# Optimization experiments

Measured on AMD Instinct MI355X. Metric: run time of the kernel, lower is better.

The kernel has to match this reference:

```python
import jax, jax.numpy as jnp
import numpy as np

B, P, V, E, F = 4, 8, 2048, 2048, 4096
BIG = 1e10  # stand-in for +inf that keeps gradients clean


def setup_inputs() -> dict:
    key = jax.random.key(0)
    ks = jax.random.split(key, 8)
    xs = jax.random.normal(ks[0], (B, V, 3), jnp.float32)
    # Projection matrices: random rows for x/y, third (depth) row kept near
    # [0,0,0,2] so the perspective divide is well conditioned for randn verts.
    pm = 0.5 * jax.random.normal(ks[1], (P, 3, 4), jnp.float32)
    pm = pm.at[:, 2, :3].set(0.01 * jax.random.normal(ks[2], (P, 3), jnp.float32))
    pm = pm.at[:, 2, 3].set(2.0)
    edgemaps = jax.random.normal(ks[3], (B, P, E, 2), jnp.float32)
    edgemap_lengths = jax.random.randint(ks[4], (B, P), E // 2, E + 1)
    boundary_mask = jax.random.randint(ks[5], (B, P, V), 0, 2).astype(bool)
    faces = jax.random.randint(ks[6], (B, F, 3), 0, V)
    target_volumes = 10.0 * jax.random.normal(ks[7], (B,), jnp.float32)
    return dict(xs=xs, projmatrices=pm, edgemaps=edgemaps,
                edgemap_lengths=edgemap_lengths, boundary_mask=boundary_mask,
                faces=faces, target_volumes=target_volumes)


def _silhouette_chamfer(xs, projmatrices, edgemaps, edgemap_lengths, boundary_mask):
    b, v, _ = xs.shape
    xh = jnp.concatenate([xs, jnp.ones((b, v, 1), xs.dtype)], axis=-1)  # [B,V,4]
    proj = jnp.einsum('pij,bvj->bpvi', projmatrices, xh)               # [B,P,V,3]
    pts = proj[..., :2] / proj[..., 2:3]                               # [B,P,V,2]
    e = edgemaps.shape[2]
    d2 = (jnp.sum(pts * pts, -1)[..., :, None]
          + jnp.sum(edgemaps * edgemaps, -1)[..., None, :]
          - 2.0 * jnp.einsum('bpvc,bpec->bpve', pts, edgemaps))
    yvalid = jnp.arange(e)[None, None, :] < edgemap_lengths[..., None]  # [B,P,E]
    d2 = jnp.where(yvalid[:, :, None, :], d2, jnp.asarray(BIG, d2.dtype))
    mins = jnp.min(d2, axis=-1)                                        # [B,P,V]
    xm = boundary_mask.astype(d2.dtype)
    # point_reduction='mean' over valid boundary points per projection,
    # batch_reduction='mean' over the P projections of each mesh.
    per_proj = jnp.sum(mins * xm, -1) / jnp.maximum(jnp.sum(xm, -1), 1.0)  # [B,P]
    return jnp.mean(per_proj, axis=-1)                                 # [B]


def _volume_constraint(xs, faces, target_volumes):
    b = xs.shape[0]
    fv = xs[jnp.arange(b)[:, None, None], faces]   # [B,F,3,3] gather face verts
    v0, v1, v2 = fv[:, :, 0], fv[:, :, 1], fv[:, :, 2]
    face_vols = jnp.sum(jnp.cross(v0, v1) * v2, axis=-1) / 6.0  # [B,F]
    vols = jnp.abs(jnp.sum(face_vols, axis=-1))                 # scatter-add per mesh
    return (vols - target_volumes) ** 2                          # [B]


def reference(xs, projmatrices, edgemaps, edgemap_lengths, boundary_mask, faces, target_volumes):
    chamfer = _silhouette_chamfer(xs, projmatrices, edgemaps, edgemap_lengths, boundary_mask)
    vol_error = _volume_constraint(xs, faces, target_volumes)
    return chamfer, vol_error
```

## Files before the change

kernel.cpp:

```cpp
#include <hip/hip_runtime.h>

#define NB 4
#define NP 8
#define NV 2048
#define NE 2048
#define NF 4096
#define BIGV 1.0e10f
#define NCOMBO (NB * NP)
#define NSPAN 16
#define NVC 16
#define VC 128
#define NBLK (NCOMBO * NVC)
#define SSTRIDE 132
#define PPAD 132


typedef float f32x2 __attribute__((ext_vector_type(2)));

__device__ __forceinline__ f32x2 pk_fma(f32x2 a, f32x2 b, f32x2 c) {
    f32x2 d;
    asm("v_pk_fma_f32 %0, %1, %2, %3" : "=v"(d) : "v"(a), "v"(b), "v"(c));
    return d;
}

__global__ __launch_bounds__(256) void fused_all(
    const float* __restrict__ xs, const float* __restrict__ pm,
    const float* __restrict__ edgemaps, const int* __restrict__ elen,
    const int* __restrict__ faces, const void* __restrict__ maskp,
    float* __restrict__ spart, float* __restrict__ cpart,
    float* __restrict__ volpart)
{
    __shared__ __align__(16) float s_ex[NSPAN * SSTRIDE];
    __shared__ __align__(16) float s_ey[NSPAN * SSTRIDE];
    __shared__ __align__(16) float s_e2[NSPAN * SSTRIDE];
    __shared__ __align__(16) float part[NSPAN * PPAD];
    __shared__ float reds[2], redc[2];
    const int tid = threadIdx.x;
    const int bid = blockIdx.x;
    const int combo  = bid >> 4;
    const int vchunk = bid & 15;
    const int b = combo >> 3;
    const int p = combo & 7;

    const int len = elen[combo];
    const float4* emapf4 = (const float4*)(edgemaps + (size_t)combo * NE * 2);
    #pragma unroll
    for (int j = 0; j < 2; j++) {
        const int q = tid + (j << 8);
        const float4 f0 = emapf4[2 * q];
        const float4 f1 = emapf4[2 * q + 1];
        float ex[4] = { f0.x, f0.z, f1.x, f1.z };
        float ey[4] = { f0.y, f0.w, f1.y, f1.w };
        float e2[4];
        const int e0 = q << 2;
        #pragma unroll
        for (int k = 0; k < 4; k++) {
            if (e0 + k < len) {
                e2[k] = ex[k] * ex[k] + ey[k] * ey[k];
            } else {
                ex[k] = 0.0f; ey[k] = 0.0f; e2[k] = BIGV;
            }
        }
        const int sp = q >> 5, pr = (q & 31) << 2;
        *(float4*)&s_ex[sp * SSTRIDE + pr] = make_float4(ex[0], ex[1], ex[2], ex[3]);
        *(float4*)&s_ey[sp * SSTRIDE + pr] = make_float4(ey[0], ey[1], ey[2], ey[3]);
        *(float4*)&s_e2[sp * SSTRIDE + pr] = make_float4(e2[0], e2[1], e2[2], e2[3]);
    }

    const float* M = pm + p * 12;
    const float m00 = M[0], m01 = M[1], m02 = M[2],  m03 = M[3];
    const float m10 = M[4], m11 = M[5], m12 = M[6],  m13 = M[7];
    const float m20 = M[8], m21 = M[9], m22 = M[10], m23 = M[11];

    const int vgroup = tid & 15;
    const int span   = tid >> 4;
    const int v0     = vchunk * VC + (vgroup << 3);

    float c24[24];
    {
        const float4* xv = (const float4*)(xs + ((size_t)b * NV + v0) * 3);
        #pragma unroll
        for (int j = 0; j < 6; j++) ((float4*)c24)[j] = xv[j];
    }
    f32x2 px2[8], py2[8];
    float v2[8], mn[8];
    #pragma unroll
    for (int i = 0; i < 8; i++) {
        const float x = c24[3 * i], y = c24[3 * i + 1], z = c24[3 * i + 2];
        const float r0 = m00 * x + m01 * y + m02 * z + m03;
        const float r1 = m10 * x + m11 * y + m12 * z + m13;
        const float r2 = m20 * x + m21 * y + m22 * z + m23;
        const float inv = 1.0f / r2;
        const float px = r0 * inv;
        const float py = r1 * inv;
        const float ax = -2.0f * px, ay = -2.0f * py;
        px2[i].x = ax; px2[i].y = ax;
        py2[i].x = ay; py2[i].y = ay;
        v2[i]  = px * px + py * py;
        mn[i]  = 3.0e38f;
    }

    float fvol = 0.0f;
    if (tid < 32) {
        const int f = (bid << 5) + tid;
        const int* fc = faces + (size_t)f * 3;
        const int i0 = fc[0], i1 = fc[1], i2 = fc[2];
        const float* xb = xs + (size_t)(f >> 12) * NV * 3;
        const float ax = xb[i0 * 3], ay = xb[i0 * 3 + 1], az = xb[i0 * 3 + 2];
        const float bx = xb[i1 * 3], by = xb[i1 * 3 + 1], bz = xb[i1 * 3 + 2];
        const float cx = xb[i2 * 3], cy = xb[i2 * 3 + 1], cz = xb[i2 * 3 + 2];
        const float crx = ay * bz - az * by;
        const float cry = az * bx - ax * bz;
        const float crz = ax * by - ay * bx;
        fvol = (crx * cx + cry * cy + crz * cz) * (1.0f / 6.0f);
    }
    __syncthreads();

    const float* bx = s_ex + span * SSTRIDE;
    const float* by = s_ey + span * SSTRIDE;
    const float* b2 = s_e2 + span * SSTRIDE;
    #pragma unroll 2
    for (int k = 0; k < 32; k++) {
        const float4 ex4 = *(const float4*)(bx + 4 * k);
        const float4 ey4 = *(const float4*)(by + 4 * k);
        const float4 e24 = *(const float4*)(b2 + 4 * k);
        f32x2 exA, exB, eyA, eyB, e2A, e2B;
        exA.x = ex4.x; exA.y = ex4.y;  exB.x = ex4.z; exB.y = ex4.w;
        eyA.x = ey4.x; eyA.y = ey4.y;  eyB.x = ey4.z; eyB.y = ey4.w;
        e2A.x = e24.x; e2A.y = e24.y;  e2B.x = e24.z; e2B.y = e24.w;
        #pragma unroll
        for (int i = 0; i < 8; i++) {
            const f32x2 dA = pk_fma(py2[i], eyA, pk_fma(px2[i], exA, e2A));
            const f32x2 dB = pk_fma(py2[i], eyB, pk_fma(px2[i], exB, e2B));
            mn[i] = fminf(fminf(mn[i], dA.x), dA.y);
            mn[i] = fminf(fminf(mn[i], dB.x), dB.y);
        }
    }

    #pragma unroll
    for (int i = 0; i < 8; i++)
        part[span * PPAD + (vgroup << 3) + i] = mn[i] + v2[i];

    const unsigned* mw = (const unsigned*)maskp;
    bool as_int = true;
    #pragma unroll
    for (int k = 0; k < 16; k++)
        if (mw[k] > 1u) as_int = false;

    __syncthreads();
    float s = 0.0f, c = 0.0f;
    if (tid < VC) {
        float m = part[tid];
        #pragma unroll
        for (int sp = 1; sp < NSPAN; sp++)
            m = fminf(m, part[sp * PPAD + tid]);
        const size_t mix = (size_t)combo * NV + vchunk * VC + tid;
        const float msk = as_int ? (((const int*)maskp)[mix] ? 1.0f : 0.0f)
                                 : (((const unsigned char*)maskp)[mix] ? 1.0f : 0.0f);
        s = m * msk;
        c = msk;
    }
    #pragma unroll
    for (int off = 32; off > 0; off >>= 1) {
        s += __shfl_down(s, off);
        c += __shfl_down(c, off);
    }
    if (tid < VC && (tid & 63) == 0) { reds[tid >> 6] = s; redc[tid >> 6] = c; }

    #pragma unroll
    for (int off = 32; off > 0; off >>= 1) fvol += __shfl_down(fvol, off);

    __syncthreads();
    if (tid == 0) {
        spart[bid]   = reds[0] + reds[1];
        cpart[bid]   = redc[0] + redc[1];
        volpart[bid] = fvol;
    }
}

__global__ __launch_bounds__(256) void finalize_k(
    const float* __restrict__ spart, const float* __restrict__ cpart,
    const float* __restrict__ volpart, const float* __restrict__ tv,
    float* __restrict__ out)
{
    __shared__ float pc[NCOMBO];
    __shared__ float rv[4];
    const int tid = threadIdx.x;
    if (tid < NCOMBO) {
        const float4* s4 = (const float4*)(spart + (tid << 4));
        const float4* c4 = (const float4*)(cpart + (tid << 4));
        float S = 0.0f, C = 0.0f;
        #pragma unroll
        for (int j = 0; j < 4; j++) {
            const float4 a = s4[j], d = c4[j];
            S += (a.x + a.y) + (a.z + a.w);
            C += (d.x + d.y) + (d.z + d.w);
        }
        pc[tid] = S / fmaxf(C, 1.0f);
    }
    const int w = tid >> 6, lane = tid & 63;
    float vs = volpart[(w << 7) + lane] + volpart[(w << 7) + 64 + lane];
    #pragma unroll
    for (int off = 32; off > 0; off >>= 1) vs += __shfl_down(vs, off);
    if (lane == 0) rv[w] = vs;
    __syncthreads();
    if (tid < NB) {
        float a = 0.0f;
        #pragma unroll
        for (int q = 0; q < NP; q++) a += pc[tid * NP + q];
        out[tid] = a * (1.0f / NP);
        const float d = fabsf(rv[tid]) - tv[tid];
        out[4 + tid] = d * d;
    }
}

extern "C" void kernel_launch(void* const* d_in, const int* in_sizes, int n_in,
                              void* d_out, int out_size, void* d_ws, size_t ws_size,
                              hipStream_t stream)
{
    const float* xs       = (const float*)d_in[0];
    const float* pm       = (const float*)d_in[1];
    const float* edgemaps = (const float*)d_in[2];
    const int*   elen     = (const int*)d_in[3];
    const void*  mask     = d_in[4];
    const int*   faces    = (const int*)d_in[5];
    const float* tv       = (const float*)d_in[6];
    float* out = (float*)d_out;

    float* spart   = (float*)d_ws;
    float* cpart   = spart + NBLK;
    float* volpart = cpart + NBLK;

    fused_all<<<dim3(NBLK), dim3(256), 0, stream>>>(
        xs, pm, edgemaps, elen, faces, mask, spart, cpart, volpart);
    finalize_k<<<dim3(1), dim3(256), 0, stream>>>(spart, cpart, volpart, tv, out);
}
```

Baseline: 77.24 us.

## Give each thread 16 vertices and fuse finalize via last-block atomic counter

Each thread now holds 16 projected vertices instead of 8 and scans a 64-edge span, with 32 spans per block instead of 16. Each shared-memory edge load is therefore reused across twice as many vertices. The squared norm is recomputed from the stored packed values rather than kept in registers, and partial minima are written to shared memory with float4 stores. The separate finalize kernel is replaced by a last-block-done pattern: a global atomic counter, zeroed by a memset before launch, lets the final block run the reduction. The trade-offs are higher register and shared-memory use per block, which may lower occupancy, plus the extra memset and fence overhead.

Result: slower. 115.5 us (+49.5%).

```diff
diff --git a/kernel.cpp b/kernel.cpp
--- a/kernel.cpp
+++ b/kernel.cpp
@@ -7,11 +7,13 @@
 #define NF 4096
 #define BIGV 1.0e10f
 #define NCOMBO (NB * NP)
-#define NSPAN 16
+#define NSPAN 32
+#define NVG 8
+#define VPT 16
 #define NVC 16
 #define VC 128
 #define NBLK (NCOMBO * NVC)
-#define SSTRIDE 132
+#define SSTRIDE 68
 #define PPAD 132
 
 
@@ -23,18 +25,56 @@
     return d;
 }
 
+__device__ __forceinline__ void finalize_out(
+    const float* __restrict__ spart, const float* __restrict__ cpart,
+    const float* __restrict__ volpart, const float* __restrict__ tv,
+    float* __restrict__ out, const int tid)
+{
+    __shared__ float pc[NCOMBO];
+    __shared__ float rv[4];
+    if (tid < NCOMBO) {
+        const float4* s4 = (const float4*)(spart + (tid << 4));
+        const float4* c4 = (const float4*)(cpart + (tid << 4));
+        float S = 0.0f, C = 0.0f;
+        #pragma unroll
+        for (int j = 0; j < 4; j++) {
+            const float4 a = s4[j], d = c4[j];
+            S += (a.x + a.y) + (a.z + a.w);
+            C += (d.x + d.y) + (d.z + d.w);
+        }
+        pc[tid] = S / fmaxf(C, 1.0f);
+    }
+    const int w = tid >> 6, lane = tid & 63;
+    float vs = volpart[(w << 7) + lane] + volpart[(w << 7) + 64 + lane];
+    #pragma unroll
+    for (int off = 32; off > 0; off >>= 1) vs += __shfl_down(vs, off);
+    if (lane == 0) rv[w] = vs;
+    __syncthreads();
+    if (tid < NB) {
+        float a = 0.0f;
+        #pragma unroll
+        for (int q = 0; q < NP; q++) a += pc[tid * NP + q];
+        out[tid] = a * (1.0f / NP);
+        const float d = fabsf(rv[tid]) - tv[tid];
+        out[4 + tid] = d * d;
+    }
+}
+
 __global__ __launch_bounds__(256) void fused_all(
     const float* __restrict__ xs, const float* __restrict__ pm,
     const float* __restrict__ edgemaps, const int* __restrict__ elen,
     const int* __restrict__ faces, const void* __restrict__ maskp,
+    const float* __restrict__ tv,
     float* __restrict__ spart, float* __restrict__ cpart,
-    float* __restrict__ volpart)
+    float* __restrict__ volpart, unsigned* __restrict__ counter,
+    float* __restrict__ out)
 {
     __shared__ __align__(16) float s_ex[NSPAN * SSTRIDE];
     __shared__ __align__(16) float s_ey[NSPAN * SSTRIDE];
     __shared__ __align__(16) float s_e2[NSPAN * SSTRIDE];
     __shared__ __align__(16) float part[NSPAN * PPAD];
     __shared__ float reds[2], redc[2];
+    __shared__ bool s_last;
     const int tid = threadIdx.x;
     const int bid = blockIdx.x;
     const int combo  = bid >> 4;
@@ -61,7 +101,7 @@
                 ex[k] = 0.0f; ey[k] = 0.0f; e2[k] = BIGV;
             }
         }
-        const int sp = q >> 5, pr = (q & 31) << 2;
+        const int sp = q >> 4, pr = (q & 15) << 2;
         *(float4*)&s_ex[sp * SSTRIDE + pr] = make_float4(ex[0], ex[1], ex[2], ex[3]);
         *(float4*)&s_ey[sp * SSTRIDE + pr] = make_float4(ey[0], ey[1], ey[2], ey[3]);
         *(float4*)&s_e2[sp * SSTRIDE + pr] = make_float4(e2[0], e2[1], e2[2], e2[3]);
@@ -72,32 +112,30 @@
     const float m10 = M[4], m11 = M[5], m12 = M[6],  m13 = M[7];
     const float m20 = M[8], m21 = M[9], m22 = M[10], m23 = M[11];
 
-    const int vgroup = tid & 15;
-    const int span   = tid >> 4;
-    const int v0     = vchunk * VC + (vgroup << 3);
-
-    float c24[24];
+    const int vg   = tid & 7;
+    const int span = tid >> 3;
+    const int v0   = vchunk * VC + vg * VPT;
+
+    float c48[48];
     {
         const float4* xv = (const float4*)(xs + ((size_t)b * NV + v0) * 3);
         #pragma unroll
-        for (int j = 0; j < 6; j++) ((float4*)c24)[j] = xv[j];
-    }
-    f32x2 px2[8], py2[8];
-    float v2[8], mn[8];
-    #pragma unroll
-    for (int i = 0; i < 8; i++) {
-        const float x = c24[3 * i], y = c24[3 * i + 1], z = c24[3 * i + 2];
+        for (int j = 0; j < 12; j++) ((float4*)c48)[j] = xv[j];
+    }
+    f32x2 px2[VPT], py2[VPT];
+    float mn[VPT];
+    #pragma unroll
+    for (int i = 0; i < VPT; i++) {
+        const float x = c48[3 * i], y = c48[3 * i + 1], z = c48[3 * i + 2];
         const float r0 = m00 * x + m01 * y + m02 * z + m03;
         const float r1 = m10 * x + m11 * y + m12 * z + m13;
         const float r2 = m20 * x + m21 * y + m22 * z + m23;
         const float inv = 1.0f / r2;
-        const float px = r0 * inv;
-        const float py = r1 * inv;
-        const float ax = -2.0f * px, ay = -2.0f * py;
+        const float ax = -2.0f * (r0 * inv);
+        const float ay = -2.0f * (r1 * inv);
         px2[i].x = ax; px2[i].y = ax;
         py2[i].x = ay; py2[i].y = ay;
-        v2[i]  = px * px + py * py;
-        mn[i]  = 3.0e38f;
+        mn[i] = 3.0e38f;
     }
 
     float fvol = 0.0f;
@@ -120,7 +158,7 @@
     const float* by = s_ey + span * SSTRIDE;
     const float* b2 = s_e2 + span * SSTRIDE;
     #pragma unroll 2
-    for (int k = 0; k < 32; k++) {
+    for (int k = 0; k < 16; k++) {
         const float4 ex4 = *(const float4*)(bx + 4 * k);
         const float4 ey4 = *(const float4*)(by + 4 * k);
         const float4 e24 = *(const float4*)(b2 + 4 * k);
@@ -129,7 +167,7 @@
         eyA.x = ey4.x; eyA.y = ey4.y;  eyB.x = ey4.z; eyB.y = ey4.w;
         e2A.x = e24.x; e2A.y = e24.y;  e2B.x = e24.z; e2B.y = e24.w;
         #pragma unroll
-        for (int i = 0; i < 8; i++) {
+        for (int i = 0; i < VPT; i++) {
             const f32x2 dA = pk_fma(py2[i], eyA, pk_fma(px2[i], exA, e2A));
             const f32x2 dB = pk_fma(py2[i], eyB, pk_fma(px2[i], exB, e2B));
             mn[i] = fminf(fminf(mn[i], dA.x), dA.y);
@@ -137,9 +175,18 @@
         }
     }
 
-    #pragma unroll
-    for (int i = 0; i < 8; i++)
-        part[span * PPAD + (vgroup << 3) + i] = mn[i] + v2[i];
+    {
+        float val[VPT];
+        #pragma unroll
+        for (int i = 0; i < VPT; i++) {
+            const float ax = px2[i].x, ay = py2[i].x;
+            const float v2 = 0.25f * fmaf(ax, ax, ay * ay);
+            val[i] = mn[i] + v2;
+        }
+        float* dst = part + span * PPAD + vg * VPT;
+        #pragma unroll
+        for (int j = 0; j < 4; j++) *(float4*)(dst + 4 * j) = ((float4*)val)[j];
+    }
 
     const unsigned* mw = (const unsigned*)maskp;
     bool as_int = true;
@@ -176,41 +223,16 @@
         cpart[bid]   = redc[0] + redc[1];
         volpart[bid] = fvol;
     }
-}
-
-__global__ __launch_bounds__(256) void finalize_k(
-    const float* __restrict__ spart, const float* __restrict__ cpart,
-    const float* __restrict__ volpart, const float* __restrict__ tv,
-    float* __restrict__ out)
-{
-    __shared__ float pc[NCOMBO];
-    __shared__ float rv[4];
-    const int tid = threadIdx.x;
-    if (tid < NCOMBO) {
-        const float4* s4 = (const float4*)(spart + (tid << 4));
-        const float4* c4 = (const float4*)(cpart + (tid << 4));
-        float S = 0.0f, C = 0.0f;
-        #pragma unroll
-        for (int j = 0; j < 4; j++) {
-            const float4 a = s4[j], d = c4[j];
-            S += (a.x + a.y) + (a.z + a.w);
-            C += (d.x + d.y) + (d.z + d.w);
-        }
-        pc[tid] = S / fmaxf(C, 1.0f);
-    }
-    const int w = tid >> 6, lane = tid & 63;
-    float vs = volpart[(w << 7) + lane] + volpart[(w << 7) + 64 + lane];
-    #pragma unroll
-    for (int off = 32; off > 0; off >>= 1) vs += __shfl_down(vs, off);
-    if (lane == 0) rv[w] = vs;
-    __syncthreads();
-    if (tid < NB) {
-        float a = 0.0f;
-        #pragma unroll
-        for (int q = 0; q < NP; q++) a += pc[tid * NP + q];
-        out[tid] = a * (1.0f / NP);
-        const float d = fabsf(rv[tid]) - tv[tid];
-        out[4 + tid] = d * d;
+
+    __threadfence();
+    if (tid == 0) {
+        const unsigned old = atomicAdd(counter, 1u);
+        s_last = (old == NBLK - 1);
+    }
+    __syncthreads();
+    if (s_last) {
+        __threadfence();
+        finalize_out(spart, cpart, volpart, tv, out, tid);
     }
 }
 
@@ -227,11 +249,12 @@
     const float* tv       = (const float*)d_in[6];
     float* out = (float*)d_out;
 
-    float* spart   = (float*)d_ws;
-    float* cpart   = spart + NBLK;
-    float* volpart = cpart + NBLK;
-
+    float*    spart   = (float*)d_ws;
+    float*    cpart   = spart + NBLK;
+    float*    volpart = cpart + NBLK;
+    unsigned* counter = (unsigned*)(volpart + NBLK);
+
+    hipMemsetAsync(counter, 0, sizeof(unsigned), stream);
     fused_all<<<dim3(NBLK), dim3(256), 0, stream>>>(
-        xs, pm, edgemaps, elen, faces, mask, spart, cpart, volpart);
-    finalize_k<<<dim3(1), dim3(256), 0, stream>>>(spart, cpart, volpart, tv, out);
-}
+        xs, pm, edgemaps, elen, faces, mask, tv, spart, cpart, volpart, counter, out);
+}
```
